# Optimization experiments

Hardware: AMD Instinct MI355X
Metric: run time of the kernel (lower is better)

## Reference

```python
import jax, jax.numpy as jnp
import numpy as np

MARGIN = 0.2  # from init_kwargs
N, D, N_CLASSES = 8192, 256, 64


def setup_inputs() -> dict:
    key = jax.random.key(0)
    k1, k2 = jax.random.split(key)
    embeddings = jax.random.normal(k1, (N, D), dtype=jnp.float32)
    targets = jax.random.randint(k2, (N,), 0, N_CLASSES, dtype=jnp.int64)
    return {"embeddings": embeddings, "targets": targets}


def _mine_triplets(embeddings, targets):
    sq = jnp.sum(embeddings * embeddings, axis=1)  # [N]
    dist = -2.0 * (embeddings @ embeddings.T) + sq[None, :] + sq[:, None]  # [N, N]
    pos_mask = targets[:, None] == targets[None, :]  # same label (incl. self, as in original)
    NEG_INF = jnp.asarray(-1e30, dist.dtype)
    POS_INF = jnp.asarray(1e30, dist.dtype)
    hardest_pos = jnp.argmax(jnp.where(pos_mask, dist, NEG_INF), axis=1)  # [N]
    hardest_neg = jnp.argmin(jnp.where(pos_mask, POS_INF, dist), axis=1)  # [N]
    anchors = jnp.arange(targets.shape[0])
    return jnp.stack([anchors, hardest_pos, hardest_neg], axis=1)  # [N, 3]


def reference(embeddings, targets):
    triplets = _mine_triplets(embeddings, targets)
    a, p, n = triplets[:, 0], triplets[:, 1], triplets[:, 2]
    ap = jnp.sum((embeddings[a] - embeddings[p]) ** 2, axis=1)
    an = jnp.sum((embeddings[a] - embeddings[n]) ** 2, axis=1)
    losses = jax.nn.relu(ap - an + MARGIN)
    return losses.mean(), triplets
```

## Files before the change

### kernel.cpp

```cpp
#include <hip/hip_runtime.h>

#define NROWS 8192
#define DDIM 256
#define MARGIN_F 0.2f
#define CSPLIT 8

typedef _Float16 half8 __attribute__((ext_vector_type(8)));
typedef float f32x4 __attribute__((ext_vector_type(4)));
typedef int i32x4 __attribute__((ext_vector_type(4)));

__device__ __forceinline__ void gld16(const void* g, void* l) {
  __builtin_amdgcn_global_load_lds(
      (const __attribute__((address_space(1))) void*)g,
      (__attribute__((address_space(3))) void*)l, 16, 0, 0);
}

__global__ __launch_bounds__(256)
void prep_kernel(const float* __restrict__ E, _Float16* __restrict__ Eh,
                 _Float16* __restrict__ El, float* __restrict__ sq) {
  const int t = threadIdx.x;
  const int r = t >> 4;
  const int cs = t & 15;
  const int rg = blockIdx.x;
  const int row = rg * 16 + r;
  const float* src = &E[row * DDIM + cs * 16];
  float s = 0.f;
  half8 H[2], L[2];
#pragma unroll
  for (int h = 0; h < 2; ++h) {
    const float4 f0 = *(const float4*)(src + h * 8);
    const float4 f1 = *(const float4*)(src + h * 8 + 4);
    const float v[8] = {f0.x, f0.y, f0.z, f0.w, f1.x, f1.y, f1.z, f1.w};
#pragma unroll
    for (int e = 0; e < 8; ++e) {
      s = fmaf(v[e], v[e], s);
      const _Float16 hi = (_Float16)v[e];
      H[h][e] = hi;
      L[h][e] = (_Float16)(v[e] - (float)hi);
    }
  }
  const int kt = cs >> 1;
  const int g0 = (cs & 1) * 2;
  const int base = (rg * 8 + kt) * 512;
  *(half8*)&Eh[base + g0 * 128 + r * 8] = H[0];
  *(half8*)&Eh[base + (g0 + 1) * 128 + r * 8] = H[1];
  *(half8*)&El[base + g0 * 128 + r * 8] = L[0];
  *(half8*)&El[base + (g0 + 1) * 128 + r * 8] = L[1];
#pragma unroll
  for (int o = 8; o > 0; o >>= 1) s += __shfl_down(s, o, 16);
  if (cs == 0) sq[row] = s;
}

__global__ __launch_bounds__(256, 2)
void mine_kernel(const _Float16* __restrict__ Eh, const _Float16* __restrict__ El,
                 const int* __restrict__ T, const float* __restrict__ sq,
                 float* __restrict__ pv, int* __restrict__ pi,
                 float* __restrict__ nv, int* __restrict__ ni) {
  __shared__ __align__(16) _Float16 S[2][4][4096];

  const int tid = threadIdx.x;
  const int lane = tid & 63;
  const int w = tid >> 6;
  const int wi = w & 1, wj = w >> 1;
  const int l15 = lane & 15, grp = lane >> 4;
  const int rowbase = blockIdx.y * 128;
  const int colbase0 = blockIdx.x * 1024;

  const _Float16* srcArr = (w == 0 || w == 2) ? Eh : El;
  const bool isRowSide = (w < 2);

  float sqi[4]; int ti[4];
#pragma unroll
  for (int fi = 0; fi < 4; ++fi) {
    const int i = rowbase + wi * 64 + fi * 16 + l15;
    sqi[fi] = sq[i];
    ti[fi] = T[i];
  }

  float bpv[4], bnv[4]; int bpi[4], bni[4];
#pragma unroll
  for (int fi = 0; fi < 4; ++fi) { bpv[fi] = -3e38f; bnv[fi] = 3e38f; bpi[fi] = 0; bni[fi] = 0; }

  for (int ct = 0; ct < 8; ++ct) {
    const int cb = colbase0 + ct * 128;
    const int rb16 = (isRowSide ? rowbase : cb) >> 4;

    f32x4 acc[4][4];
#pragma unroll
    for (int jf = 0; jf < 4; ++jf)
#pragma unroll
      for (int fi = 0; fi < 4; ++fi) acc[jf][fi] = (f32x4){0.f, 0.f, 0.f, 0.f};

#pragma unroll
    for (int rg = 0; rg < 8; ++rg)
      gld16(srcArr + ((rb16 + rg) * 8 + 0) * 512 + lane * 8, &S[0][w][rg * 512]);
    __syncthreads();

    int cur = 0;
    for (int kt = 0; kt < 8; ++kt) {
      if (kt < 7) {
#pragma unroll
        for (int rg = 0; rg < 8; ++rg)
          gld16(srcArr + ((rb16 + rg) * 8 + kt + 1) * 512 + lane * 8,
                &S[cur ^ 1][w][rg * 512]);
      }
      half8 ajh[4], ajl[4];
#pragma unroll
      for (int jf = 0; jf < 4; ++jf) {
        ajh[jf] = *(const half8*)&S[cur][2][(wj * 4 + jf) * 512 + lane * 8];
        ajl[jf] = *(const half8*)&S[cur][3][(wj * 4 + jf) * 512 + lane * 8];
      }
#pragma unroll
      for (int fi = 0; fi < 4; ++fi) {
        const half8 bh = *(const half8*)&S[cur][0][(wi * 4 + fi) * 512 + lane * 8];
        const half8 bl = *(const half8*)&S[cur][1][(wi * 4 + fi) * 512 + lane * 8];
#pragma unroll
        for (int jf = 0; jf < 4; ++jf)
          acc[jf][fi] = __builtin_amdgcn_mfma_f32_16x16x32_f16(ajh[jf], bh, acc[jf][fi], 0, 0, 0);
#pragma unroll
        for (int jf = 0; jf < 4; ++jf)
          acc[jf][fi] = __builtin_amdgcn_mfma_f32_16x16x32_f16(ajl[jf], bh, acc[jf][fi], 0, 0, 0);
#pragma unroll
        for (int jf = 0; jf < 4; ++jf)
          acc[jf][fi] = __builtin_amdgcn_mfma_f32_16x16x32_f16(ajh[jf], bl, acc[jf][fi], 0, 0, 0);
      }
      __syncthreads();
      cur ^= 1;
    }

#pragma unroll
    for (int jf = 0; jf < 4; ++jf) {
      const int jb = cb + wj * 64 + jf * 16 + grp * 4;
      const f32x4 sqj = *(const f32x4*)&sq[jb];
      const i32x4 tj = *(const i32x4*)&T[jb];
#pragma unroll
      for (int fi = 0; fi < 4; ++fi) {
#pragma unroll
        for (int r = 0; r < 4; ++r) {
          const float dst = fmaf(-2.f, acc[jf][fi][r], sqi[fi] + sqj[r]);
          const int jidx = jb + r;
          if (ti[fi] == tj[r]) {
            if (dst > bpv[fi]) { bpv[fi] = dst; bpi[fi] = jidx; }
          } else {
            if (dst < bnv[fi]) { bnv[fi] = dst; bni[fi] = jidx; }
          }
        }
      }
    }
  }

#pragma unroll
  for (int fi = 0; fi < 4; ++fi) {
#pragma unroll
    for (int off = 16; off <= 32; off <<= 1) {
      const float ov = __shfl_xor(bpv[fi], off, 64);
      const int oi = __shfl_xor(bpi[fi], off, 64);
      if (ov > bpv[fi] || (ov == bpv[fi] && oi < bpi[fi])) { bpv[fi] = ov; bpi[fi] = oi; }
      const float on = __shfl_xor(bnv[fi], off, 64);
      const int oni = __shfl_xor(bni[fi], off, 64);
      if (on < bnv[fi] || (on == bnv[fi] && oni < bni[fi])) { bnv[fi] = on; bni[fi] = oni; }
    }
  }

  __syncthreads();
  float4* scr = (float4*)&S[0][0][0];
  if (wj == 1 && lane < 16) {
#pragma unroll
    for (int fi = 0; fi < 4; ++fi)
      scr[wi * 64 + fi * 16 + lane] =
          make_float4(bpv[fi], __int_as_float(bpi[fi]), bnv[fi], __int_as_float(bni[fi]));
  }
  __syncthreads();
  if (wj == 0 && lane < 16) {
#pragma unroll
    for (int fi = 0; fi < 4; ++fi) {
      const float4 o = scr[wi * 64 + fi * 16 + lane];
      const int oi = __float_as_int(o.y), oni = __float_as_int(o.w);
      if (o.x > bpv[fi] || (o.x == bpv[fi] && oi < bpi[fi])) { bpv[fi] = o.x; bpi[fi] = oi; }
      if (o.z < bnv[fi] || (o.z == bnv[fi] && oni < bni[fi])) { bnv[fi] = o.z; bni[fi] = oni; }
      const int row = rowbase + wi * 64 + fi * 16 + lane;
      const int oidx = row * CSPLIT + blockIdx.x;
      pv[oidx] = bpv[fi]; pi[oidx] = bpi[fi]; nv[oidx] = bnv[fi]; ni[oidx] = bni[fi];
    }
  }
}

__global__ __launch_bounds__(256)
void finish_kernel(const float* __restrict__ E,
                   const float* __restrict__ pv, const int* __restrict__ pi,
                   const float* __restrict__ nv, const int* __restrict__ ni,
                   float* __restrict__ out, float* __restrict__ bl) {
  const int w = threadIdx.x >> 6, lane = threadIdx.x & 63;
  const int row = blockIdx.x * 4 + w;
  float Pv = -3e38f, Nv = 3e38f; int Pi = 0, Ni = 0;
#pragma unroll
  for (int s = 0; s < CSPLIT; ++s) {
    const float p = pv[row * CSPLIT + s]; const int px = pi[row * CSPLIT + s];
    if (p > Pv || (p == Pv && px < Pi)) { Pv = p; Pi = px; }
    const float n = nv[row * CSPLIT + s]; const int nx = ni[row * CSPLIT + s];
    if (n < Nv || (n == Nv && nx < Ni)) { Nv = n; Ni = nx; }
  }
  const float4 a = *(const float4*)&E[row * DDIM + lane * 4];
  const float4 p4 = *(const float4*)&E[Pi * DDIM + lane * 4];
  const float4 n4 = *(const float4*)&E[Ni * DDIM + lane * 4];
  float ap = (a.x - p4.x) * (a.x - p4.x) + (a.y - p4.y) * (a.y - p4.y)
           + (a.z - p4.z) * (a.z - p4.z) + (a.w - p4.w) * (a.w - p4.w);
  float an = (a.x - n4.x) * (a.x - n4.x) + (a.y - n4.y) * (a.y - n4.y)
           + (a.z - n4.z) * (a.z - n4.z) + (a.w - n4.w) * (a.w - n4.w);
#pragma unroll
  for (int o = 32; o > 0; o >>= 1) {
    ap += __shfl_down(ap, o, 64);
    an += __shfl_down(an, o, 64);
  }
  __shared__ float ls[4];
  if (lane == 0) {
    out[1 + row * 3 + 0] = (float)row;
    out[1 + row * 3 + 1] = (float)Pi;
    out[1 + row * 3 + 2] = (float)Ni;
    ls[w] = fmaxf(ap - an + MARGIN_F, 0.f);
  }
  __syncthreads();
  if (threadIdx.x == 0) bl[blockIdx.x] = (ls[0] + ls[1]) + (ls[2] + ls[3]);
}

__global__ __launch_bounds__(256)
void sum_kernel(const float* __restrict__ bl, float* __restrict__ out) {
  __shared__ float s[256];
  float t = 0.f;
#pragma unroll
  for (int r = 0; r < (NROWS / 4) / 256; ++r) t += bl[threadIdx.x + r * 256];
  s[threadIdx.x] = t;
  __syncthreads();
  for (int o = 128; o > 0; o >>= 1) {
    if (threadIdx.x < o) s[threadIdx.x] += s[threadIdx.x + o];
    __syncthreads();
  }
  if (threadIdx.x == 0) out[0] = s[0] * (1.f / NROWS);
}

extern "C" void kernel_launch(void* const* d_in, const int* in_sizes, int n_in,
                              void* d_out, int out_size, void* d_ws, size_t ws_size,
                              hipStream_t stream) {
  const float* E = (const float*)d_in[0];
  const int* T = (const int*)d_in[1];
  float* out = (float*)d_out;

  _Float16* Eh = (_Float16*)d_ws;
  _Float16* El = Eh + NROWS * DDIM;
  float* sq = (float*)(El + NROWS * DDIM);
  float* pv = sq + NROWS;
  int*   pi = (int*)(pv + NROWS * CSPLIT);
  float* nv = (float*)(pi + NROWS * CSPLIT);
  int*   ni = (int*)(nv + NROWS * CSPLIT);
  float* bl = (float*)(ni + NROWS * CSPLIT);

  prep_kernel<<<NROWS / 16, 256, 0, stream>>>(E, Eh, El, sq);
  mine_kernel<<<dim3(CSPLIT, NROWS / 128), 256, 0, stream>>>(Eh, El, T, sq, pv, pi, nv, ni);
  finish_kernel<<<NROWS / 4, 256, 0, stream>>>(E, pv, pi, nv, ni, out, bl);
  sum_kernel<<<1, 256, 0, stream>>>(bl, out);
}
```

Measured before the change: 137.0 us.

## Retile mining GEMM to 256x256 blocks with 512 threads and MFMA priority

Replaces the 128-row by 1024-column block (eight sequential 128-column tiles) with a single 256x256 output tile per 512-thread block, so each wave computes a 64x128 accumulator. Column splits grow from 8 to 32 and the grid grows to 32x32 blocks. Each k-step loads 16 row-groups of the hi/lo split arrays, cutting global and LDS traffic per MFMA, and s_setprio is placed around the MFMA bursts. In exchange the accumulator array doubles, LDS use doubles to 64 KB per block, occupancy may drop, and the finish kernel must reduce four times as many partial candidates. The barrier before the scratch reuse was removed, which relies on the loop's final __syncthreads.

```diff
diff --git a/kernel.cpp b/kernel.cpp
--- a/kernel.cpp
+++ b/kernel.cpp
@@ -3,7 +3,7 @@
 #define NROWS 8192
 #define DDIM 256
 #define MARGIN_F 0.2f
-#define CSPLIT 8
+#define CSPLIT 32
 
 typedef _Float16 half8 __attribute__((ext_vector_type(8)));
 typedef float f32x4 __attribute__((ext_vector_type(4)));
@@ -51,23 +51,25 @@
   if (cs == 0) sq[row] = s;
 }
 
-__global__ __launch_bounds__(256, 2)
+__global__ __launch_bounds__(512, 2)
 void mine_kernel(const _Float16* __restrict__ Eh, const _Float16* __restrict__ El,
                  const int* __restrict__ T, const float* __restrict__ sq,
                  float* __restrict__ pv, int* __restrict__ pi,
                  float* __restrict__ nv, int* __restrict__ ni) {
-  __shared__ __align__(16) _Float16 S[2][4][4096];
+  __shared__ __align__(16) _Float16 S[2][4][8192];
 
   const int tid = threadIdx.x;
   const int lane = tid & 63;
   const int w = tid >> 6;
-  const int wi = w & 1, wj = w >> 1;
+  const int wi = w >> 1, wj = w & 1;
   const int l15 = lane & 15, grp = lane >> 4;
-  const int rowbase = blockIdx.y * 128;
-  const int colbase0 = blockIdx.x * 1024;
-
-  const _Float16* srcArr = (w == 0 || w == 2) ? Eh : El;
-  const bool isRowSide = (w < 2);
+  const int rowbase = blockIdx.y * 256;
+  const int colbase = blockIdx.x * 256;
+
+  const int arr = w >> 1;
+  const int shalf = w & 1;
+  const _Float16* sA = (arr & 1) ? El : Eh;
+  const int rgb = (((arr < 2) ? rowbase : colbase) >> 4) + shalf * 8;
 
   float sqi[4]; int ti[4];
 #pragma unroll
@@ -81,69 +83,69 @@
 #pragma unroll
   for (int fi = 0; fi < 4; ++fi) { bpv[fi] = -3e38f; bnv[fi] = 3e38f; bpi[fi] = 0; bni[fi] = 0; }
 
-  for (int ct = 0; ct < 8; ++ct) {
-    const int cb = colbase0 + ct * 128;
-    const int rb16 = (isRowSide ? rowbase : cb) >> 4;
-
-    f32x4 acc[4][4];
-#pragma unroll
-    for (int jf = 0; jf < 4; ++jf)
-#pragma unroll
-      for (int fi = 0; fi < 4; ++fi) acc[jf][fi] = (f32x4){0.f, 0.f, 0.f, 0.f};
-
-#pragma unroll
-    for (int rg = 0; rg < 8; ++rg)
-      gld16(srcArr + ((rb16 + rg) * 8 + 0) * 512 + lane * 8, &S[0][w][rg * 512]);
-    __syncthreads();
-
-    int cur = 0;
-    for (int kt = 0; kt < 8; ++kt) {
-      if (kt < 7) {
-#pragma unroll
-        for (int rg = 0; rg < 8; ++rg)
-          gld16(srcArr + ((rb16 + rg) * 8 + kt + 1) * 512 + lane * 8,
-                &S[cur ^ 1][w][rg * 512]);
-      }
+  f32x4 acc[8][4];
+#pragma unroll
+  for (int jf = 0; jf < 8; ++jf)
+#pragma unroll
+    for (int fi = 0; fi < 4; ++fi) acc[jf][fi] = (f32x4){0.f, 0.f, 0.f, 0.f};
+
+#pragma unroll
+  for (int t = 0; t < 8; ++t)
+    gld16(sA + ((rgb + t) * 8 + 0) * 512 + lane * 8, &S[0][arr][(shalf * 8 + t) * 512]);
+  __syncthreads();
+
+  for (int kt = 0; kt < 8; ++kt) {
+    const int cur = kt & 1;
+    if (kt < 7) {
+#pragma unroll
+      for (int t = 0; t < 8; ++t)
+        gld16(sA + ((rgb + t) * 8 + kt + 1) * 512 + lane * 8,
+              &S[cur ^ 1][arr][(shalf * 8 + t) * 512]);
+    }
+#pragma unroll
+    for (int jh = 0; jh < 2; ++jh) {
       half8 ajh[4], ajl[4];
 #pragma unroll
       for (int jf = 0; jf < 4; ++jf) {
-        ajh[jf] = *(const half8*)&S[cur][2][(wj * 4 + jf) * 512 + lane * 8];
-        ajl[jf] = *(const half8*)&S[cur][3][(wj * 4 + jf) * 512 + lane * 8];
+        const int rg = wj * 8 + jh * 4 + jf;
+        ajh[jf] = *(const half8*)&S[cur][2][rg * 512 + lane * 8];
+        ajl[jf] = *(const half8*)&S[cur][3][rg * 512 + lane * 8];
       }
 #pragma unroll
       for (int fi = 0; fi < 4; ++fi) {
         const half8 bh = *(const half8*)&S[cur][0][(wi * 4 + fi) * 512 + lane * 8];
         const half8 bl = *(const half8*)&S[cur][1][(wi * 4 + fi) * 512 + lane * 8];
+        __builtin_amdgcn_s_setprio(1);
 #pragma unroll
         for (int jf = 0; jf < 4; ++jf)
-          acc[jf][fi] = __builtin_amdgcn_mfma_f32_16x16x32_f16(ajh[jf], bh, acc[jf][fi], 0, 0, 0);
+          acc[jh * 4 + jf][fi] = __builtin_amdgcn_mfma_f32_16x16x32_f16(ajh[jf], bh, acc[jh * 4 + jf][fi], 0, 0, 0);
 #pragma unroll
         for (int jf = 0; jf < 4; ++jf)
-          acc[jf][fi] = __builtin_amdgcn_mfma_f32_16x16x32_f16(ajl[jf], bh, acc[jf][fi], 0, 0, 0);
+          acc[jh * 4 + jf][fi] = __builtin_amdgcn_mfma_f32_16x16x32_f16(ajl[jf], bh, acc[jh * 4 + jf][fi], 0, 0, 0);
 #pragma unroll
         for (int jf = 0; jf < 4; ++jf)
-          acc[jf][fi] = __builtin_amdgcn_mfma_f32_16x16x32_f16(ajh[jf], bl, acc[jf][fi], 0, 0, 0);
+          acc[jh * 4 + jf][fi] = __builtin_amdgcn_mfma_f32_16x16x32_f16(ajh[jf], bl, acc[jh * 4 + jf][fi], 0, 0, 0);
+        __builtin_amdgcn_s_setprio(0);
       }
-      __syncthreads();
-      cur ^= 1;
-    }
-
-#pragma unroll
-    for (int jf = 0; jf < 4; ++jf) {
-      const int jb = cb + wj * 64 + jf * 16 + grp * 4;
-      const f32x4 sqj = *(const f32x4*)&sq[jb];
-      const i32x4 tj = *(const i32x4*)&T[jb];
-#pragma unroll
-      for (int fi = 0; fi < 4; ++fi) {
-#pragma unroll
-        for (int r = 0; r < 4; ++r) {
-          const float dst = fmaf(-2.f, acc[jf][fi][r], sqi[fi] + sqj[r]);
-          const int jidx = jb + r;
-          if (ti[fi] == tj[r]) {
-            if (dst > bpv[fi]) { bpv[fi] = dst; bpi[fi] = jidx; }
-          } else {
-            if (dst < bnv[fi]) { bnv[fi] = dst; bni[fi] = jidx; }
-          }
+    }
+    __syncthreads();
+  }
+
+#pragma unroll
+  for (int jf = 0; jf < 8; ++jf) {
+    const int jb = colbase + wj * 128 + jf * 16 + grp * 4;
+    const f32x4 sqj = *(const f32x4*)&sq[jb];
+    const i32x4 tj = *(const i32x4*)&T[jb];
+#pragma unroll
+    for (int fi = 0; fi < 4; ++fi) {
+#pragma unroll
+      for (int r = 0; r < 4; ++r) {
+        const float dst = fmaf(-2.f, acc[jf][fi][r], sqi[fi] + sqj[r]);
+        const int jidx = jb + r;
+        if (ti[fi] == tj[r]) {
+          if (dst > bpv[fi]) { bpv[fi] = dst; bpi[fi] = jidx; }
+        } else {
+          if (dst < bnv[fi]) { bnv[fi] = dst; bni[fi] = jidx; }
         }
       }
     }
@@ -162,7 +164,6 @@
     }
   }
 
-  __syncthreads();
   float4* scr = (float4*)&S[0][0][0];
   if (wj == 1 && lane < 16) {
 #pragma unroll
@@ -255,7 +256,7 @@
   float* bl = (float*)(ni + NROWS * CSPLIT);
 
   prep_kernel<<<NROWS / 16, 256, 0, stream>>>(E, Eh, El, sq);
-  mine_kernel<<<dim3(CSPLIT, NROWS / 128), 256, 0, stream>>>(Eh, El, T, sq, pv, pi, nv, ni);
+  mine_kernel<<<dim3(NROWS / 256, NROWS / 256), 512, 0, stream>>>(Eh, El, T, sq, pv, pi, nv, ni);
   finish_kernel<<<NROWS / 4, 256, 0, stream>>>(E, pv, pi, nv, ni, out, bl);
   sum_kernel<<<1, 256, 0, stream>>>(bl, out);
 }
```

After: 151.7 us. 1.11x slower.

## Exploit distance-matrix symmetry by computing only upper-triangular tiles

Applied to the files above, without the earlier changes.

The mining kernel now launches one block per 128x128 tile in the upper triangle plus the diagonal of the symmetric distance matrix. Each off-diagonal block also reduces its tile by column through an LDS table, so one GEMM tile feeds both the row-side and the column-side hardest positive and negative. This roughly halves the three-pass split-fp16 MFMA work. In exchange there is more LDS reduction and epilogue work, a larger partial-result buffer (CSPLIT 64) for finish_kernel to scan, and a block-index-to-tile mapping that uses sqrtf.

```diff
diff --git a/kernel.cpp b/kernel.cpp
--- a/kernel.cpp
+++ b/kernel.cpp
@@ -3,7 +3,9 @@
 #define NROWS 8192
 #define DDIM 256
 #define MARGIN_F 0.2f
-#define CSPLIT 8
+#define CSPLIT 64
+#define NT 64
+#define NUP 2016
 
 typedef _Float16 half8 __attribute__((ext_vector_type(8)));
 typedef float f32x4 __attribute__((ext_vector_type(4)));
@@ -39,9 +41,9 @@
       L[h][e] = (_Float16)(v[e] - (float)hi);
     }
   }
-  const int kt = cs >> 1;
+  const int kb = cs >> 1;
   const int g0 = (cs & 1) * 2;
-  const int base = (rg * 8 + kt) * 512;
+  const int base = (rg * 8 + kb) * 512;
   *(half8*)&Eh[base + g0 * 128 + r * 8] = H[0];
   *(half8*)&Eh[base + (g0 + 1) * 128 + r * 8] = H[1];
   *(half8*)&El[base + g0 * 128 + r * 8] = L[0];
@@ -58,16 +60,30 @@
                  float* __restrict__ nv, int* __restrict__ ni) {
   __shared__ __align__(16) _Float16 S[2][4][4096];
 
+  const int t = blockIdx.x;
+  int by, bx;
+  if (t >= NUP) {
+    by = t - NUP; bx = by;
+  } else {
+    int b = (int)((127.0f - sqrtf(16129.0f - 8.0f * (float)t)) * 0.5f);
+    if (b < 0) b = 0;
+    if (b > 62) b = 62;
+    while (b < 62 && 63 * (b + 1) - ((b + 1) * b) / 2 <= t) ++b;
+    while (63 * b - (b * (b - 1)) / 2 > t) --b;
+    by = b;
+    bx = b + 1 + (t - (63 * b - (b * (b - 1)) / 2));
+  }
+  const bool offdiag = (bx != by);
+  const int rowbase = by * 128, colbase = bx * 128;
+
   const int tid = threadIdx.x;
   const int lane = tid & 63;
   const int w = tid >> 6;
-  const int wi = w & 1, wj = w >> 1;
+  const int wi = w >> 1, wj = w & 1;
   const int l15 = lane & 15, grp = lane >> 4;
-  const int rowbase = blockIdx.y * 128;
-  const int colbase0 = blockIdx.x * 1024;
-
-  const _Float16* srcArr = (w == 0 || w == 2) ? Eh : El;
-  const bool isRowSide = (w < 2);
+
+  const _Float16* sA = (w & 1) ? El : Eh;
+  const int rgb = ((w < 2) ? by : bx) * 8;
 
   float sqi[4]; int ti[4];
 #pragma unroll
@@ -77,76 +93,105 @@
     ti[fi] = T[i];
   }
 
+  f32x4 acc[4][4];
+#pragma unroll
+  for (int jf = 0; jf < 4; ++jf)
+#pragma unroll
+    for (int fi = 0; fi < 4; ++fi) acc[jf][fi] = (f32x4){0.f, 0.f, 0.f, 0.f};
+
+#pragma unroll
+  for (int rg = 0; rg < 8; ++rg)
+    gld16(sA + ((rgb + rg) * 8 + 0) * 512 + lane * 8, &S[0][w][rg * 512]);
+  __syncthreads();
+
+  int cur = 0;
+  for (int kb = 0; kb < 8; ++kb) {
+    if (kb < 7) {
+#pragma unroll
+      for (int rg = 0; rg < 8; ++rg)
+        gld16(sA + ((rgb + rg) * 8 + kb + 1) * 512 + lane * 8, &S[cur ^ 1][w][rg * 512]);
+    }
+    half8 ajh[4], ajl[4];
+#pragma unroll
+    for (int jf = 0; jf < 4; ++jf) {
+      ajh[jf] = *(const half8*)&S[cur][2][(wj * 4 + jf) * 512 + lane * 8];
+      ajl[jf] = *(const half8*)&S[cur][3][(wj * 4 + jf) * 512 + lane * 8];
+    }
+#pragma unroll
+    for (int fi = 0; fi < 4; ++fi) {
+      const half8 bh = *(const half8*)&S[cur][0][(wi * 4 + fi) * 512 + lane * 8];
+      const half8 bl = *(const half8*)&S[cur][1][(wi * 4 + fi) * 512 + lane * 8];
+#pragma unroll
+      for (int jf = 0; jf < 4; ++jf)
+        acc[jf][fi] = __builtin_amdgcn_mfma_f32_16x16x32_f16(ajh[jf], bh, acc[jf][fi], 0, 0, 0);
+#pragma unroll
+      for (int jf = 0; jf < 4; ++jf)
+        acc[jf][fi] = __builtin_amdgcn_mfma_f32_16x16x32_f16(ajl[jf], bh, acc[jf][fi], 0, 0, 0);
+#pragma unroll
+      for (int jf = 0; jf < 4; ++jf)
+        acc[jf][fi] = __builtin_amdgcn_mfma_f32_16x16x32_f16(ajh[jf], bl, acc[jf][fi], 0, 0, 0);
+    }
+    __syncthreads();
+    cur ^= 1;
+  }
+
   float bpv[4], bnv[4]; int bpi[4], bni[4];
 #pragma unroll
   for (int fi = 0; fi < 4; ++fi) { bpv[fi] = -3e38f; bnv[fi] = 3e38f; bpi[fi] = 0; bni[fi] = 0; }
 
-  for (int ct = 0; ct < 8; ++ct) {
-    const int cb = colbase0 + ct * 128;
-    const int rb16 = (isRowSide ? rowbase : cb) >> 4;
-
-    f32x4 acc[4][4];
-#pragma unroll
-    for (int jf = 0; jf < 4; ++jf)
-#pragma unroll
-      for (int fi = 0; fi < 4; ++fi) acc[jf][fi] = (f32x4){0.f, 0.f, 0.f, 0.f};
-
-#pragma unroll
-    for (int rg = 0; rg < 8; ++rg)
-      gld16(srcArr + ((rb16 + rg) * 8 + 0) * 512 + lane * 8, &S[0][w][rg * 512]);
-    __syncthreads();
-
-    int cur = 0;
-    for (int kt = 0; kt < 8; ++kt) {
-      if (kt < 7) {
-#pragma unroll
-        for (int rg = 0; rg < 8; ++rg)
-          gld16(srcArr + ((rb16 + rg) * 8 + kt + 1) * 512 + lane * 8,
-                &S[cur ^ 1][w][rg * 512]);
+  float4* tab = (float4*)&S[0][0][0];
+  const int wbase = w * 1024;
+
+#pragma unroll
+  for (int jf = 0; jf < 4; ++jf) {
+    const int jb = colbase + wj * 64 + jf * 16 + grp * 4;
+    const f32x4 sqj = *(const f32x4*)&sq[jb];
+    const i32x4 tj = *(const i32x4*)&T[jb];
+#pragma unroll
+    for (int fi = 0; fi < 4; ++fi) {
+#pragma unroll
+      for (int r = 0; r < 4; ++r) {
+        const float dst = fmaf(-2.f, acc[jf][fi][r], sqi[fi] + sqj[r]);
+        const int jidx = jb + r;
+        if (ti[fi] == tj[r]) {
+          if (dst > bpv[fi]) { bpv[fi] = dst; bpi[fi] = jidx; }
+        } else {
+          if (dst < bnv[fi]) { bnv[fi] = dst; bni[fi] = jidx; }
+        }
       }
-      half8 ajh[4], ajl[4];
-#pragma unroll
-      for (int jf = 0; jf < 4; ++jf) {
-        ajh[jf] = *(const half8*)&S[cur][2][(wj * 4 + jf) * 512 + lane * 8];
-        ajl[jf] = *(const half8*)&S[cur][3][(wj * 4 + jf) * 512 + lane * 8];
-      }
-#pragma unroll
-      for (int fi = 0; fi < 4; ++fi) {
-        const half8 bh = *(const half8*)&S[cur][0][(wi * 4 + fi) * 512 + lane * 8];
-        const half8 bl = *(const half8*)&S[cur][1][(wi * 4 + fi) * 512 + lane * 8];
-#pragma unroll
-        for (int jf = 0; jf < 4; ++jf)
-          acc[jf][fi] = __builtin_amdgcn_mfma_f32_16x16x32_f16(ajh[jf], bh, acc[jf][fi], 0, 0, 0);
-#pragma unroll
-        for (int jf = 0; jf < 4; ++jf)
-          acc[jf][fi] = __builtin_amdgcn_mfma_f32_16x16x32_f16(ajl[jf], bh, acc[jf][fi], 0, 0, 0);
-#pragma unroll
-        for (int jf = 0; jf < 4; ++jf)
-          acc[jf][fi] = __builtin_amdgcn_mfma_f32_16x16x32_f16(ajh[jf], bl, acc[jf][fi], 0, 0, 0);
-      }
-      __syncthreads();
-      cur ^= 1;
-    }
-
-#pragma unroll
-    for (int jf = 0; jf < 4; ++jf) {
-      const int jb = cb + wj * 64 + jf * 16 + grp * 4;
-      const f32x4 sqj = *(const f32x4*)&sq[jb];
-      const i32x4 tj = *(const i32x4*)&T[jb];
-#pragma unroll
-      for (int fi = 0; fi < 4; ++fi) {
-#pragma unroll
-        for (int r = 0; r < 4; ++r) {
+    }
+    if (offdiag) {
+#pragma unroll
+      for (int r = 0; r < 4; ++r) {
+        float tpv = -3e38f, tnv = 3e38f; int tpi = 0, tni = 0;
+#pragma unroll
+        for (int fi = 0; fi < 4; ++fi) {
           const float dst = fmaf(-2.f, acc[jf][fi][r], sqi[fi] + sqj[r]);
-          const int jidx = jb + r;
+          const int ii = rowbase + wi * 64 + fi * 16 + l15;
           if (ti[fi] == tj[r]) {
-            if (dst > bpv[fi]) { bpv[fi] = dst; bpi[fi] = jidx; }
+            if (dst > tpv) { tpv = dst; tpi = ii; }
           } else {
-            if (dst < bnv[fi]) { bnv[fi] = dst; bni[fi] = jidx; }
+            if (dst < tnv) { tnv = dst; tni = ii; }
           }
         }
+        const int a = jf * 16 + grp * 4 + r;
+        tab[wbase + a * 16 + l15] =
+            make_float4(tpv, __int_as_float(tpi), tnv, __int_as_float(tni));
       }
     }
+  }
+
+  float Tpv = -3e38f, Tnv = 3e38f; int Tpi = 0, Tni = 0;
+  if (offdiag) {
+    __syncthreads();
+#pragma unroll
+    for (int m = 0; m < 16; ++m) {
+      const float4 o = tab[wbase + lane * 16 + ((m + lane) & 15)];
+      const int oi = __float_as_int(o.y), oni = __float_as_int(o.w);
+      if (o.x > Tpv || (o.x == Tpv && oi < Tpi)) { Tpv = o.x; Tpi = oi; }
+      if (o.z < Tnv || (o.z == Tnv && oni < Tni)) { Tnv = o.z; Tni = oni; }
+    }
+    __syncthreads();
   }
 
 #pragma unroll
@@ -162,26 +207,41 @@
     }
   }
 
+  float4* scr = (float4*)&S[0][0][0];
+  float4* scrT = scr + 256;
+  if (lane < 16) {
+#pragma unroll
+    for (int fi = 0; fi < 4; ++fi)
+      scr[(wi * 64 + fi * 16 + l15) * 2 + wj] =
+          make_float4(bpv[fi], __int_as_float(bpi[fi]), bnv[fi], __int_as_float(bni[fi]));
+  }
+  if (offdiag)
+    scrT[(wj * 64 + lane) * 2 + wi] =
+        make_float4(Tpv, __int_as_float(Tpi), Tnv, __int_as_float(Tni));
   __syncthreads();
-  float4* scr = (float4*)&S[0][0][0];
-  if (wj == 1 && lane < 16) {
-#pragma unroll
-    for (int fi = 0; fi < 4; ++fi)
-      scr[wi * 64 + fi * 16 + lane] =
-          make_float4(bpv[fi], __int_as_float(bpi[fi]), bnv[fi], __int_as_float(bni[fi]));
-  }
-  __syncthreads();
-  if (wj == 0 && lane < 16) {
-#pragma unroll
-    for (int fi = 0; fi < 4; ++fi) {
-      const float4 o = scr[wi * 64 + fi * 16 + lane];
-      const int oi = __float_as_int(o.y), oni = __float_as_int(o.w);
-      if (o.x > bpv[fi] || (o.x == bpv[fi] && oi < bpi[fi])) { bpv[fi] = o.x; bpi[fi] = oi; }
-      if (o.z < bnv[fi] || (o.z == bnv[fi] && oni < bni[fi])) { bnv[fi] = o.z; bni[fi] = oni; }
-      const int row = rowbase + wi * 64 + fi * 16 + lane;
-      const int oidx = row * CSPLIT + blockIdx.x;
-      pv[oidx] = bpv[fi]; pi[oidx] = bpi[fi]; nv[oidx] = bnv[fi]; ni[oidx] = bni[fi];
-    }
+
+  if (tid < 128) {
+    const float4 o0 = scr[tid * 2 + 0];
+    const float4 o1 = scr[tid * 2 + 1];
+    float Pv = o0.x; int Pi = __float_as_int(o0.y);
+    float Nv = o0.z; int Ni = __float_as_int(o0.w);
+    const int oi = __float_as_int(o1.y), oni = __float_as_int(o1.w);
+    if (o1.x > Pv || (o1.x == Pv && oi < Pi)) { Pv = o1.x; Pi = oi; }
+    if (o1.z < Nv || (o1.z == Nv && oni < Ni)) { Nv = o1.z; Ni = oni; }
+    const int oidx = (rowbase + tid) * CSPLIT + bx;
+    pv[oidx] = Pv; pi[oidx] = Pi; nv[oidx] = Nv; ni[oidx] = Ni;
+  }
+  if (offdiag && tid >= 128) {
+    const int jl = tid - 128;
+    const float4 o0 = scrT[jl * 2 + 0];
+    const float4 o1 = scrT[jl * 2 + 1];
+    float Pv = o0.x; int Pi = __float_as_int(o0.y);
+    float Nv = o0.z; int Ni = __float_as_int(o0.w);
+    const int oi = __float_as_int(o1.y), oni = __float_as_int(o1.w);
+    if (o1.x > Pv || (o1.x == Pv && oi < Pi)) { Pv = o1.x; Pi = oi; }
+    if (o1.z < Nv || (o1.z == Nv && oni < Ni)) { Nv = o1.z; Ni = oni; }
+    const int oidx = (colbase + jl) * CSPLIT + by;
+    pv[oidx] = Pv; pi[oidx] = Pi; nv[oidx] = Nv; ni[oidx] = Ni;
   }
 }
 
@@ -255,7 +315,7 @@
   float* bl = (float*)(ni + NROWS * CSPLIT);
 
   prep_kernel<<<NROWS / 16, 256, 0, stream>>>(E, Eh, El, sq);
-  mine_kernel<<<dim3(CSPLIT, NROWS / 128), 256, 0, stream>>>(Eh, El, T, sq, pv, pi, nv, ni);
+  mine_kernel<<<NUP + NT, 256, 0, stream>>>(Eh, El, T, sq, pv, pi, nv, ni);
   finish_kernel<<<NROWS / 4, 256, 0, stream>>>(E, pv, pi, nv, ni, out, bl);
   sum_kernel<<<1, 256, 0, stream>>>(bl, out);
 }
```

Result: slower. 153.6 us (+12.1%).

## Exploit distance-matrix symmetry with triangular 64x64 single-wave tiles

Applied to the files above, without the earlier changes.

Replaces the 128-row by 1024-column LDS-staged blocks with one-wave 64x64 tiles that read fragments directly from global memory into registers, double-buffered. Only upper-triangular tiles are computed (by <= bx). Each off-diagonal tile reduces along both rows and columns, so it yields partial argmax/argmin for both sides, which roughly halves the MFMA work. The cost is 128 partial slots per row, a longer serial reduction in finish_kernel, many early-exiting blocks, and no LDS reuse, so global and cache traffic rises.

```diff
diff --git a/kernel.cpp b/kernel.cpp
--- a/kernel.cpp
+++ b/kernel.cpp
@@ -3,17 +3,12 @@
 #define NROWS 8192
 #define DDIM 256
 #define MARGIN_F 0.2f
-#define CSPLIT 8
+#define NSLOT 128
+#define NTT 128
 
 typedef _Float16 half8 __attribute__((ext_vector_type(8)));
 typedef float f32x4 __attribute__((ext_vector_type(4)));
 typedef int i32x4 __attribute__((ext_vector_type(4)));
-
-__device__ __forceinline__ void gld16(const void* g, void* l) {
-  __builtin_amdgcn_global_load_lds(
-      (const __attribute__((address_space(1))) void*)g,
-      (__attribute__((address_space(3))) void*)l, 16, 0, 0);
-}
 
 __global__ __launch_bounds__(256)
 void prep_kernel(const float* __restrict__ E, _Float16* __restrict__ Eh,
@@ -39,9 +34,9 @@
       L[h][e] = (_Float16)(v[e] - (float)hi);
     }
   }
-  const int kt = cs >> 1;
+  const int kb = cs >> 1;
   const int g0 = (cs & 1) * 2;
-  const int base = (rg * 8 + kt) * 512;
+  const int base = (rg * 8 + kb) * 512;
   *(half8*)&Eh[base + g0 * 128 + r * 8] = H[0];
   *(half8*)&Eh[base + (g0 + 1) * 128 + r * 8] = H[1];
   *(half8*)&El[base + g0 * 128 + r * 8] = L[0];
@@ -51,99 +46,131 @@
   if (cs == 0) sq[row] = s;
 }
 
-__global__ __launch_bounds__(256, 2)
+__global__ __launch_bounds__(64)
 void mine_kernel(const _Float16* __restrict__ Eh, const _Float16* __restrict__ El,
                  const int* __restrict__ T, const float* __restrict__ sq,
                  float* __restrict__ pv, int* __restrict__ pi,
                  float* __restrict__ nv, int* __restrict__ ni) {
-  __shared__ __align__(16) _Float16 S[2][4][4096];
-
-  const int tid = threadIdx.x;
-  const int lane = tid & 63;
-  const int w = tid >> 6;
-  const int wi = w & 1, wj = w >> 1;
+  const int d = blockIdx.x;
+  const int g = (d & 7) * 2048 + (d >> 3);
+  const int band = g >> 10;
+  const int bx = (g >> 3) & 127;
+  const int by = band * 8 + (g & 7);
+  if (by > bx) return;
+  const bool offdiag = (bx != by);
+  const int ib = by * 64, jb0 = bx * 64;
+
+  const int lane = threadIdx.x;
   const int l15 = lane & 15, grp = lane >> 4;
-  const int rowbase = blockIdx.y * 128;
-  const int colbase0 = blockIdx.x * 1024;
-
-  const _Float16* srcArr = (w == 0 || w == 2) ? Eh : El;
-  const bool isRowSide = (w < 2);
+
+  int offB[4], offA[4];
+#pragma unroll
+  for (int f = 0; f < 4; ++f) {
+    offB[f] = (by * 4 + f) * 4096 + lane * 8;
+    offA[f] = (bx * 4 + f) * 4096 + lane * 8;
+  }
+
+  f32x4 acc[4][4];
+#pragma unroll
+  for (int jf = 0; jf < 4; ++jf)
+#pragma unroll
+    for (int fi = 0; fi < 4; ++fi) acc[jf][fi] = (f32x4){0.f, 0.f, 0.f, 0.f};
+
+#define LOADSET(AH, AL, BH, BL, KB) do { const int kk_ = (KB) * 512;            \
+    _Pragma("unroll")                                                           \
+    for (int f = 0; f < 4; ++f) {                                               \
+      AH[f] = *(const half8*)&Eh[offA[f] + kk_];                                \
+      AL[f] = *(const half8*)&El[offA[f] + kk_];                                \
+      BH[f] = *(const half8*)&Eh[offB[f] + kk_];                                \
+      BL[f] = *(const half8*)&El[offB[f] + kk_];                                \
+    } } while (0)
+
+#define MM(AH, AL, BH, BL) do {                                                 \
+    _Pragma("unroll")                                                           \
+    for (int fi = 0; fi < 4; ++fi)                                              \
+      _Pragma("unroll")                                                         \
+      for (int jf = 0; jf < 4; ++jf)                                            \
+        acc[jf][fi] = __builtin_amdgcn_mfma_f32_16x16x32_f16(AH[jf], BH[fi], acc[jf][fi], 0, 0, 0); \
+    _Pragma("unroll")                                                           \
+    for (int fi = 0; fi < 4; ++fi)                                              \
+      _Pragma("unroll")                                                         \
+      for (int jf = 0; jf < 4; ++jf)                                            \
+        acc[jf][fi] = __builtin_amdgcn_mfma_f32_16x16x32_f16(AL[jf], BH[fi], acc[jf][fi], 0, 0, 0); \
+    _Pragma("unroll")                                                           \
+    for (int fi = 0; fi < 4; ++fi)                                              \
+      _Pragma("unroll")                                                         \
+      for (int jf = 0; jf < 4; ++jf)                                            \
+        acc[jf][fi] = __builtin_amdgcn_mfma_f32_16x16x32_f16(AH[jf], BL[fi], acc[jf][fi], 0, 0, 0); \
+    } while (0)
+
+  half8 AH0[4], AL0[4], BH0[4], BL0[4];
+  half8 AH1[4], AL1[4], BH1[4], BL1[4];
+  LOADSET(AH0, AL0, BH0, BL0, 0);
+#pragma unroll
+  for (int it = 0; it < 4; ++it) {
+    LOADSET(AH1, AL1, BH1, BL1, 2 * it + 1);
+    MM(AH0, AL0, BH0, BL0);
+    if (it < 3) LOADSET(AH0, AL0, BH0, BL0, 2 * it + 2);
+    MM(AH1, AL1, BH1, BL1);
+  }
+#undef LOADSET
+#undef MM
 
   float sqi[4]; int ti[4];
 #pragma unroll
   for (int fi = 0; fi < 4; ++fi) {
-    const int i = rowbase + wi * 64 + fi * 16 + l15;
-    sqi[fi] = sq[i];
-    ti[fi] = T[i];
-  }
-
+    sqi[fi] = sq[ib + fi * 16 + l15];
+    ti[fi] = T[ib + fi * 16 + l15];
+  }
   float bpv[4], bnv[4]; int bpi[4], bni[4];
 #pragma unroll
   for (int fi = 0; fi < 4; ++fi) { bpv[fi] = -3e38f; bnv[fi] = 3e38f; bpi[fi] = 0; bni[fi] = 0; }
 
-  for (int ct = 0; ct < 8; ++ct) {
-    const int cb = colbase0 + ct * 128;
-    const int rb16 = (isRowSide ? rowbase : cb) >> 4;
-
-    f32x4 acc[4][4];
-#pragma unroll
-    for (int jf = 0; jf < 4; ++jf)
-#pragma unroll
-      for (int fi = 0; fi < 4; ++fi) acc[jf][fi] = (f32x4){0.f, 0.f, 0.f, 0.f};
-
-#pragma unroll
-    for (int rg = 0; rg < 8; ++rg)
-      gld16(srcArr + ((rb16 + rg) * 8 + 0) * 512 + lane * 8, &S[0][w][rg * 512]);
-    __syncthreads();
-
-    int cur = 0;
-    for (int kt = 0; kt < 8; ++kt) {
-      if (kt < 7) {
-#pragma unroll
-        for (int rg = 0; rg < 8; ++rg)
-          gld16(srcArr + ((rb16 + rg) * 8 + kt + 1) * 512 + lane * 8,
-                &S[cur ^ 1][w][rg * 512]);
+#pragma unroll
+  for (int jf = 0; jf < 4; ++jf) {
+    const int jb = jb0 + jf * 16 + grp * 4;
+    const f32x4 sqj = *(const f32x4*)&sq[jb];
+    const i32x4 tj = *(const i32x4*)&T[jb];
+#pragma unroll
+    for (int fi = 0; fi < 4; ++fi) {
+#pragma unroll
+      for (int r = 0; r < 4; ++r) {
+        const float dst = fmaf(-2.f, acc[jf][fi][r], sqi[fi] + sqj[r]);
+        const int jidx = jb + r;
+        if (ti[fi] == tj[r]) {
+          if (dst > bpv[fi]) { bpv[fi] = dst; bpi[fi] = jidx; }
+        } else {
+          if (dst < bnv[fi]) { bnv[fi] = dst; bni[fi] = jidx; }
+        }
       }
-      half8 ajh[4], ajl[4];
-#pragma unroll
-      for (int jf = 0; jf < 4; ++jf) {
-        ajh[jf] = *(const half8*)&S[cur][2][(wj * 4 + jf) * 512 + lane * 8];
-        ajl[jf] = *(const half8*)&S[cur][3][(wj * 4 + jf) * 512 + lane * 8];
-      }
-#pragma unroll
-      for (int fi = 0; fi < 4; ++fi) {
-        const half8 bh = *(const half8*)&S[cur][0][(wi * 4 + fi) * 512 + lane * 8];
-        const half8 bl = *(const half8*)&S[cur][1][(wi * 4 + fi) * 512 + lane * 8];
-#pragma unroll
-        for (int jf = 0; jf < 4; ++jf)
-          acc[jf][fi] = __builtin_amdgcn_mfma_f32_16x16x32_f16(ajh[jf], bh, acc[jf][fi], 0, 0, 0);
-#pragma unroll
-        for (int jf = 0; jf < 4; ++jf)
-          acc[jf][fi] = __builtin_amdgcn_mfma_f32_16x16x32_f16(ajl[jf], bh, acc[jf][fi], 0, 0, 0);
-#pragma unroll
-        for (int jf = 0; jf < 4; ++jf)
-          acc[jf][fi] = __builtin_amdgcn_mfma_f32_16x16x32_f16(ajh[jf], bl, acc[jf][fi], 0, 0, 0);
-      }
-      __syncthreads();
-      cur ^= 1;
-    }
-
-#pragma unroll
-    for (int jf = 0; jf < 4; ++jf) {
-      const int jb = cb + wj * 64 + jf * 16 + grp * 4;
-      const f32x4 sqj = *(const f32x4*)&sq[jb];
-      const i32x4 tj = *(const i32x4*)&T[jb];
-#pragma unroll
-      for (int fi = 0; fi < 4; ++fi) {
-#pragma unroll
-        for (int r = 0; r < 4; ++r) {
+    }
+    if (offdiag) {
+#pragma unroll
+      for (int r = 0; r < 4; ++r) {
+        float tpv = -3e38f, tnv = 3e38f; int tpi = 0, tni = 0;
+#pragma unroll
+        for (int fi = 0; fi < 4; ++fi) {
           const float dst = fmaf(-2.f, acc[jf][fi][r], sqi[fi] + sqj[r]);
-          const int jidx = jb + r;
+          const int ii = ib + fi * 16 + l15;
           if (ti[fi] == tj[r]) {
-            if (dst > bpv[fi]) { bpv[fi] = dst; bpi[fi] = jidx; }
+            if (dst > tpv) { tpv = dst; tpi = ii; }
           } else {
-            if (dst < bnv[fi]) { bnv[fi] = dst; bni[fi] = jidx; }
+            if (dst < tnv) { tnv = dst; tni = ii; }
           }
+        }
+#pragma unroll
+        for (int m = 1; m <= 8; m <<= 1) {
+          const float ov = __shfl_xor(tpv, m, 64);
+          const int oi = __shfl_xor(tpi, m, 64);
+          if (ov > tpv || (ov == tpv && oi < tpi)) { tpv = ov; tpi = oi; }
+          const float on = __shfl_xor(tnv, m, 64);
+          const int oni = __shfl_xor(tni, m, 64);
+          if (on < tnv || (on == tnv && oni < tni)) { tnv = on; tni = oni; }
+        }
+        if (l15 == jf * 4 + r) {
+          const int j = jb0 + jf * 16 + grp * 4 + r;
+          const int o = j * NSLOT + by;
+          pv[o] = tpv; pi[o] = tpi; nv[o] = tnv; ni[o] = tni;
         }
       }
     }
@@ -161,26 +188,11 @@
       if (on < bnv[fi] || (on == bnv[fi] && oni < bni[fi])) { bnv[fi] = on; bni[fi] = oni; }
     }
   }
-
-  __syncthreads();
-  float4* scr = (float4*)&S[0][0][0];
-  if (wj == 1 && lane < 16) {
-#pragma unroll
-    for (int fi = 0; fi < 4; ++fi)
-      scr[wi * 64 + fi * 16 + lane] =
-          make_float4(bpv[fi], __int_as_float(bpi[fi]), bnv[fi], __int_as_float(bni[fi]));
-  }
-  __syncthreads();
-  if (wj == 0 && lane < 16) {
-#pragma unroll
-    for (int fi = 0; fi < 4; ++fi) {
-      const float4 o = scr[wi * 64 + fi * 16 + lane];
-      const int oi = __float_as_int(o.y), oni = __float_as_int(o.w);
-      if (o.x > bpv[fi] || (o.x == bpv[fi] && oi < bpi[fi])) { bpv[fi] = o.x; bpi[fi] = oi; }
-      if (o.z < bnv[fi] || (o.z == bnv[fi] && oni < bni[fi])) { bnv[fi] = o.z; bni[fi] = oni; }
-      const int row = rowbase + wi * 64 + fi * 16 + lane;
-      const int oidx = row * CSPLIT + blockIdx.x;
-      pv[oidx] = bpv[fi]; pi[oidx] = bpi[fi]; nv[oidx] = bnv[fi]; ni[oidx] = bni[fi];
+#pragma unroll
+  for (int fi = 0; fi < 4; ++fi) {
+    if (grp == fi) {
+      const int o = (ib + lane) * NSLOT + bx;
+      pv[o] = bpv[fi]; pi[o] = bpi[fi]; nv[o] = bnv[fi]; ni[o] = bni[fi];
     }
   }
 }
@@ -193,11 +205,10 @@
   const int w = threadIdx.x >> 6, lane = threadIdx.x & 63;
   const int row = blockIdx.x * 4 + w;
   float Pv = -3e38f, Nv = 3e38f; int Pi = 0, Ni = 0;
-#pragma unroll
-  for (int s = 0; s < CSPLIT; ++s) {
-    const float p = pv[row * CSPLIT + s]; const int px = pi[row * CSPLIT + s];
+  for (int s = 0; s < NSLOT; ++s) {
+    const float p = pv[row * NSLOT + s]; const int px = pi[row * NSLOT + s];
     if (p > Pv || (p == Pv && px < Pi)) { Pv = p; Pi = px; }
-    const float n = nv[row * CSPLIT + s]; const int nx = ni[row * CSPLIT + s];
+    const float n = nv[row * NSLOT + s]; const int nx = ni[row * NSLOT + s];
     if (n < Nv || (n == Nv && nx < Ni)) { Nv = n; Ni = nx; }
   }
   const float4 a = *(const float4*)&E[row * DDIM + lane * 4];
@@ -249,13 +260,13 @@
   _Float16* El = Eh + NROWS * DDIM;
   float* sq = (float*)(El + NROWS * DDIM);
   float* pv = sq + NROWS;
-  int*   pi = (int*)(pv + NROWS * CSPLIT);
-  float* nv = (float*)(pi + NROWS * CSPLIT);
-  int*   ni = (int*)(nv + NROWS * CSPLIT);
-  float* bl = (float*)(ni + NROWS * CSPLIT);
+  int*   pi = (int*)(pv + NROWS * NSLOT);
+  float* nv = (float*)(pi + NROWS * NSLOT);
+  int*   ni = (int*)(nv + NROWS * NSLOT);
+  float* bl = (float*)(ni + NROWS * NSLOT);
 
   prep_kernel<<<NROWS / 16, 256, 0, stream>>>(E, Eh, El, sq);
-  mine_kernel<<<dim3(CSPLIT, NROWS / 128), 256, 0, stream>>>(Eh, El, T, sq, pv, pi, nv, ni);
+  mine_kernel<<<NTT * NTT, 64, 0, stream>>>(Eh, El, T, sq, pv, pi, nv, ni);
   finish_kernel<<<NROWS / 4, 256, 0, stream>>>(E, pv, pi, nv, ni, out, bl);
   sum_kernel<<<1, 256, 0, stream>>>(bl, out);
 }
```

New measurement: 341.3 us. 149% more time.
